# Kernel tuning notes

Hardware: AMD Instinct MI355X
Metric: run time of the kernel (lower is better)

The kernel has to match this reference:

```python
import jax, jax.numpy as jnp
import numpy as np

B, S, D = 2, 2048, 2048
NH, NKV, HD = 16, 4, 128
REP = NH // NKV
EPS = 1e-6
ROPE_THETA = 1e6


def setup_inputs() -> dict:
    key = jax.random.key(0)
    ks = jax.random.split(key, 6)
    x = jax.random.normal(ks[0], (B, S, D), jnp.float32)
    # real rotary embeddings: [S, HD]
    inv_freq = 1.0 / (ROPE_THETA ** (np.arange(0, HD, 2, dtype=np.float64) / HD))
    freqs = np.outer(np.arange(S, dtype=np.float64), inv_freq)
    emb = np.concatenate([freqs, freqs], axis=-1)
    cos = jnp.asarray(np.cos(emb), jnp.float32)
    sin = jnp.asarray(np.sin(emb), jnp.float32)
    scale = 1.0 / np.sqrt(D)
    Wq = jax.random.normal(ks[1], (D, NH * HD), jnp.float32) * scale   # [in, out]
    Wk = jax.random.normal(ks[2], (D, NKV * HD), jnp.float32) * scale
    Wv = jax.random.normal(ks[3], (D, NKV * HD), jnp.float32) * scale
    Wo = jax.random.normal(ks[4], (NH * HD, D), jnp.float32) * (1.0 / np.sqrt(NH * HD))
    q_norm_w = jnp.ones((HD,), jnp.float32)
    k_norm_w = jnp.ones((HD,), jnp.float32)
    return dict(x=x, cos=cos, sin=sin, Wq=Wq, Wk=Wk, Wv=Wv, Wo=Wo,
                q_norm_w=q_norm_w, k_norm_w=k_norm_w)


def _rms_norm(h, w):
    var = jnp.mean(h * h, axis=-1, keepdims=True)
    return w * (h * jax.lax.rsqrt(var + EPS))


def _rotate_half(h):
    h1, h2 = jnp.split(h, 2, axis=-1)
    return jnp.concatenate([-h2, h1], axis=-1)


def reference(x, cos, sin, Wq, Wk, Wv, Wo, q_norm_w, k_norm_w):
    b, s, _ = x.shape
    q = (x @ Wq).reshape(b, s, NH, HD)
    k = (x @ Wk).reshape(b, s, NKV, HD)
    v = (x @ Wv).reshape(b, s, NKV, HD)
    # per-head QK RMSNorm
    q = _rms_norm(q, q_norm_w)
    k = _rms_norm(k, k_norm_w)
    # RoPE: cos/sin [S,HD] -> broadcast over batch and heads
    c = cos[None, :, None, :]
    s_ = sin[None, :, None, :]
    q = q * c + _rotate_half(q) * s_
    k = k * c + _rotate_half(k) * s_
    # GQA: group q heads per kv head instead of materializing repeat_kv
    qg = q.reshape(b, s, NKV, REP, HD)
    scores = jnp.einsum('bqgrd,bkgd->bgrqk', qg, k) / np.sqrt(HD)
    causal = jnp.tril(jnp.ones((s, s), bool))  # [q,k]
    scores = jnp.where(causal, scores, -jnp.inf)
    probs = jax.nn.softmax(scores.astype(jnp.float32), axis=-1).astype(q.dtype)
    out = jnp.einsum('bgrqk,bkgd->bqgrd', probs, v).reshape(b, s, NH * HD)
    return out @ Wo
```

## Files before the change

### kernel.cpp

```cpp
#include <hip/hip_runtime.h>
#include <hip/hip_bf16.h>
#include <math.h>

#define B_ 2
#define S_ 2048
#define D_ 2048
#define NH_ 16
#define NKV_ 4
#define HD_ 128
#define EPS_ 1e-6f
#define SCALE_ 0.08838834764831845f
#define LOG2E_ 1.4426950408889634f
#define KOFF_ 2048
#define VOFF_ 2560

typedef float f32x4 __attribute__((ext_vector_type(4)));
typedef short bf16x8 __attribute__((ext_vector_type(8)));
typedef short short4v __attribute__((ext_vector_type(4)));
typedef float float4v __attribute__((ext_vector_type(4)));
typedef unsigned uint2v __attribute__((ext_vector_type(2)));
typedef unsigned uint4v __attribute__((ext_vector_type(4)));

static __device__ __forceinline__ short f2bf(float f) {
    union { float f; unsigned u; } x{f};
    unsigned r = (x.u + 0x7fff + ((x.u >> 16) & 1)) >> 16;
    return (short)r;
}
static __device__ __forceinline__ float bf2f(short s) {
    union { unsigned u; float f; } x; x.u = ((unsigned)(unsigned short)s) << 16; return x.f;
}
static __device__ __forceinline__ unsigned pack_bf2(float a, float b) {
    return __builtin_amdgcn_perm(__builtin_bit_cast(unsigned, b),
                                 __builtin_bit_cast(unsigned, a), 0x07060302u);
}

#define AS1(p) ((const __attribute__((address_space(1))) void*)(p))
#define AS3(p) ((__attribute__((address_space(3))) void*)(p))
static __device__ __forceinline__ void async16(const void* g, void* l) {
    __builtin_amdgcn_global_load_lds(AS1(g), AS3(l), 16, 0, 0);
}
#define SB_() __builtin_amdgcn_sched_barrier(0)

__global__ __launch_bounds__(256) void cast_kernel(const float* __restrict__ in,
                                                   short* __restrict__ out) {
    size_t i = ((size_t)blockIdx.x * 256 + threadIdx.x) * 4;
    float4v v = *(const float4v*)(in + i);
    short4v o; o.x = f2bf(v.x); o.y = f2bf(v.y); o.z = f2bf(v.z); o.w = f2bf(v.w);
    *(short4v*)(out + i) = o;
}

__global__ __launch_bounds__(256) void transpose_all_kernel(const float* __restrict__ Wq,
                                                            const float* __restrict__ Wk,
                                                            const float* __restrict__ Wv,
                                                            const float* __restrict__ Wo,
                                                            short* __restrict__ Wt,
                                                            short* __restrict__ Wot) {
    __shared__ float tile[64][65];
    const int bx = blockIdx.x, by = blockIdx.y;
    const float* src; short* dst; int N, nb;
    if (bx < 32)      { src = Wq; dst = Wt;                         N = 2048; nb = bx; }
    else if (bx < 40) { src = Wk; dst = Wt + (size_t)KOFF_ * 2048;  N = 512;  nb = bx - 32; }
    else if (bx < 48) { src = Wv; dst = Wt + (size_t)VOFF_ * 2048;  N = 512;  nb = bx - 40; }
    else              { src = Wo; dst = Wot;                        N = 2048; nb = bx - 48; }
    const int n0 = nb * 64, k0 = by * 64;
    const int tid = threadIdx.x;
    for (int r = 0; r < 16; ++r) {
        int k = r * 4 + (tid >> 6);
        int n = tid & 63;
        tile[k][n] = src[(size_t)(k0 + k) * N + n0 + n];
    }
    __syncthreads();
    for (int r = 0; r < 4; ++r) {
        int n  = r * 16 + (tid >> 4);
        int kk = (tid & 15) * 4;
        short4v o4;
        o4.x = f2bf(tile[kk + 0][n]); o4.y = f2bf(tile[kk + 1][n]);
        o4.z = f2bf(tile[kk + 2][n]); o4.w = f2bf(tile[kk + 3][n]);
        *(short4v*)&dst[(size_t)(n0 + n) * 2048 + k0 + kk] = o4;
    }
}

__global__ __launch_bounds__(512, 2) void gemm_oproj_kernel(const short* __restrict__ A,
                                                            const short* __restrict__ Bt,
                                                            float* __restrict__ C) {
    __shared__ __align__(16) short smem[49152];
    short* A0 = smem;
    short* A1 = smem + 8192;
    short* B0 = smem + 16384;
    short* B1 = smem + 32768;

    const int tid  = threadIdx.x;
    const int orig = blockIdx.y * 8 + blockIdx.x;
    const int swz  = (orig & 7) * 32 + (orig >> 3);
    const int bn = swz & 7, bm = swz >> 3;
    const int wave = tid >> 6, lane = tid & 63;
    const int quad = lane >> 4, l16 = lane & 15;
    const int wr = wave >> 2, wc = wave & 3;

    const short* Ag = A  + (size_t)(bm * 128) * 2048;
    const short* Bg = Bt + (size_t)(bn * 256) * 2048;

    f32x4 acc[4][4];
#pragma unroll
    for (int i = 0; i < 4; ++i)
#pragma unroll
        for (int j = 0; j < 4; ++j) acc[i][j] = (f32x4){0.f, 0.f, 0.f, 0.f};

    bf16x8 a[4][2], b0[2][2], b1[2][2];

    auto stage_half = [&](const short* gpanel, int t, int h, short* lslot) {
#pragma unroll
        for (int u = 0; u < 2; ++u) {
            int ci = u * 512 + tid;
            int r  = ci >> 3;
            int cb = ((ci & 7) * 16) ^ ((r & 7) << 4);
            async16(gpanel + (size_t)(h * 128 + r) * 2048 + t * 64 + (cb >> 1),
                    lslot + h * 8192 + ci * 8);
        }
    };

#define OLDA_(lbuf) \
    _Pragma("unroll") for (int mt = 0; mt < 4; ++mt) \
    _Pragma("unroll") for (int ks = 0; ks < 2; ++ks) { \
        int row_ = wr * 64 + mt * 16 + l16; \
        int cb_  = (ks * 64 + quad * 16) ^ ((row_ & 7) << 4); \
        a[mt][ks] = *(const bf16x8*)&(lbuf)[row_ * 64 + (cb_ >> 1)]; \
    }
#define OLDB_(lbuf, qn, breg) \
    _Pragma("unroll") for (int ntl = 0; ntl < 2; ++ntl) \
    _Pragma("unroll") for (int ks = 0; ks < 2; ++ks) { \
        int row_ = wc * 64 + (qn) * 32 + ntl * 16 + l16; \
        int cb_  = (ks * 64 + quad * 16) ^ ((row_ & 7) << 4); \
        breg[ntl][ks] = *(const bf16x8*)&(lbuf)[row_ * 64 + (cb_ >> 1)]; \
    }
#define OMFMA_(qn, breg) do { \
    __builtin_amdgcn_s_setprio(1); \
    _Pragma("unroll") for (int mt = 0; mt < 4; ++mt) \
    _Pragma("unroll") for (int ntl = 0; ntl < 2; ++ntl) \
    _Pragma("unroll") for (int ks = 0; ks < 2; ++ks) \
        acc[mt][(qn) * 2 + ntl] = __builtin_amdgcn_mfma_f32_16x16x32_bf16( \
            a[mt][ks], breg[ntl][ks], acc[mt][(qn) * 2 + ntl], 0, 0, 0); \
    __builtin_amdgcn_s_setprio(0); SB_(); __builtin_amdgcn_s_barrier(); } while (0)

    stage_half(Bg, 0, 0, B0); stage_half(Bg, 0, 1, B0);
    stage_half(Ag, 0, 0, A0);
    SB_(); asm volatile("s_waitcnt vmcnt(0)" ::: "memory");
    __builtin_amdgcn_s_barrier();

#pragma unroll 1
    for (int i = 0; i < 16; ++i) {
        const int tE = 2 * i, tO = 2 * i + 1;
        const bool more = (i < 15);

        stage_half(Ag, tO, 0, A1);
        stage_half(Bg, tO, 0, B1); stage_half(Bg, tO, 1, B1);
        OLDA_(A0); OLDB_(B0, 0, b0);
        OMFMA_(0, b0);

        if (more) {
            stage_half(Ag, tE + 2, 0, A0);
            SB_(); asm volatile("s_waitcnt vmcnt(2)" ::: "memory");
        } else {
            SB_(); asm volatile("s_waitcnt vmcnt(0)" ::: "memory");
        }
        OLDB_(B0, 1, b1);
        OMFMA_(1, b1);

        if (more) { stage_half(Bg, tE + 2, 0, B0); stage_half(Bg, tE + 2, 1, B0); }
        OLDA_(A1); OLDB_(B1, 0, b0);
        OMFMA_(0, b0);

        if (more) { SB_(); asm volatile("s_waitcnt vmcnt(0)" ::: "memory"); }
        OLDB_(B1, 1, b1);
        OMFMA_(1, b1);
    }

#pragma unroll
    for (int mt = 0; mt < 4; ++mt)
#pragma unroll
        for (int nt = 0; nt < 4; ++nt)
#pragma unroll
            for (int j = 0; j < 4; ++j) {
                int row = bm * 128 + wr * 64 + mt * 16 + quad * 4 + j;
                int col = bn * 256 + wc * 64 + nt * 16 + l16;
                C[(size_t)row * 2048 + col] = acc[mt][nt][j];
            }
#undef OLDA_
#undef OLDB_
#undef OMFMA_
}

#define QKV_ITERS 16

__global__ __launch_bounds__(512, 2) void qkv_fused_kernel(const short* __restrict__ xb,
                                                           const short* __restrict__ Wt,
                                                           const float* __restrict__ cosb,
                                                           const float* __restrict__ sinb,
                                                           const float* __restrict__ qw,
                                                           const float* __restrict__ kw,
                                                           short* __restrict__ q_rope,
                                                           short* __restrict__ k_rope,
                                                           short* __restrict__ vtr) {
    __shared__ __align__(16) short smem[65536];
    __shared__ float ss2[4][256];

    short* A0 = smem;
    short* A1 = smem + 16384;
    short* B0 = smem + 32768;
    short* B1 = smem + 49152;

    const int tid  = threadIdx.x;
    const int orig = blockIdx.y * 12 + blockIdx.x;
    const int swz  = (orig & 7) * 24 + (orig >> 3);
    const int bn = swz % 12, bm = swz / 12;
    const int wave = tid >> 6, lane = tid & 63;
    const int quad = lane >> 4, l16 = lane & 15;
    const int wr = wave >> 2, wc = wave & 3;

    const short* Ag = xb + (size_t)(bm * 256) * 2048;
    const short* Bg = Wt + (size_t)(bn * 256) * 2048;

    f32x4 acc[8][4];
#pragma unroll
    for (int i = 0; i < 8; ++i)
#pragma unroll
        for (int j = 0; j < 4; ++j) acc[i][j] = (f32x4){0.f, 0.f, 0.f, 0.f};

    bf16x8 a[4][2], b0[2][2], b1[2][2];

    auto stage_half = [&](const short* gpanel, int t, int h, short* lslot) {
#pragma unroll
        for (int u = 0; u < 2; ++u) {
            int ci = u * 512 + tid;
            int r  = ci >> 3;
            int cb = ((ci & 7) * 16) ^ ((r & 7) << 4);
            async16(gpanel + (size_t)(h * 128 + r) * 2048 + t * 64 + (cb >> 1),
                    lslot + h * 8192 + ci * 8);
        }
    };

#define LDA_(lbuf, qm) \
    _Pragma("unroll") for (int mt = 0; mt < 4; ++mt) \
    _Pragma("unroll") for (int ks = 0; ks < 2; ++ks) { \
        int row_ = wr * 128 + (qm) * 64 + mt * 16 + l16; \
        int cb_  = (ks * 64 + quad * 16) ^ ((row_ & 7) << 4); \
        a[mt][ks] = *(const bf16x8*)&(lbuf)[row_ * 64 + (cb_ >> 1)]; \
    }
#define LDB_(lbuf, qn, breg) \
    _Pragma("unroll") for (int ntl = 0; ntl < 2; ++ntl) \
    _Pragma("unroll") for (int ks = 0; ks < 2; ++ks) { \
        int row_ = wc * 64 + (qn) * 32 + ntl * 16 + l16; \
        int cb_  = (ks * 64 + quad * 16) ^ ((row_ & 7) << 4); \
        breg[ntl][ks] = *(const bf16x8*)&(lbuf)[row_ * 64 + (cb_ >> 1)]; \
    }
#define MFMA16_(qm, qn, breg) \
    _Pragma("unroll") for (int mt = 0; mt < 4; ++mt) \
    _Pragma("unroll") for (int ntl = 0; ntl < 2; ++ntl) \
    _Pragma("unroll") for (int ks = 0; ks < 2; ++ks) \
        acc[(qm) * 4 + mt][(qn) * 2 + ntl] = __builtin_amdgcn_mfma_f32_16x16x32_bf16( \
            a[mt][ks], breg[ntl][ks], acc[(qm) * 4 + mt][(qn) * 2 + ntl], 0, 0, 0);
#define PH_MFMA2_(qm) do { \
        __builtin_amdgcn_s_setprio(1); MFMA16_(qm, 0, b0); MFMA16_(qm, 1, b1); \
        __builtin_amdgcn_s_setprio(0); SB_(); __builtin_amdgcn_s_barrier(); } while (0)

    stage_half(Bg, 0, 0, B0); stage_half(Bg, 0, 1, B0);
    stage_half(Ag, 0, 0, A0); stage_half(Ag, 0, 1, A0);
    stage_half(Bg, 1, 0, B1); stage_half(Bg, 1, 1, B1);
    SB_(); asm volatile("s_waitcnt vmcnt(4)" ::: "memory");
    __builtin_amdgcn_s_barrier();

#pragma unroll 1
    for (int i = 0; i < QKV_ITERS; ++i) {
        const int tE = 2 * i, tO = 2 * i + 1;
        const bool more = (i < QKV_ITERS - 1);

        stage_half(Ag, tO, 0, A1); stage_half(Ag, tO, 1, A1);
        LDA_(A0, 0); LDB_(B0, 0, b0); LDB_(B0, 1, b1);
        PH_MFMA2_(0);

        if (more) {
            stage_half(Bg, tE + 2, 0, B0); stage_half(Bg, tE + 2, 1, B0);
            SB_(); asm volatile("s_waitcnt vmcnt(4)" ::: "memory");
        } else {
            SB_(); asm volatile("s_waitcnt vmcnt(0)" ::: "memory");
        }
        LDA_(A0, 1);
        PH_MFMA2_(1);

        if (more) { stage_half(Ag, tE + 2, 0, A0); stage_half(Ag, tE + 2, 1, A0); }
        LDA_(A1, 0); LDB_(B1, 0, b0); LDB_(B1, 1, b1);
        PH_MFMA2_(0);

        if (more) {
            stage_half(Bg, tO + 2, 0, B1); stage_half(Bg, tO + 2, 1, B1);
            SB_(); asm volatile("s_waitcnt vmcnt(4)" ::: "memory");
        }
        LDA_(A1, 1);
        PH_MFMA2_(1);
    }

    if (bn >= 10) {
        const int gbase = (bn - 10) * 2;
#pragma unroll
        for (int am = 0; am < 8; ++am) {
            int tok0 = bm * 256 + wr * 128 + am * 16 + quad * 4;
            int bb = tok0 >> 11, s0 = tok0 & (S_ - 1);
#pragma unroll
            for (int nt = 0; nt < 4; ++nt) {
                int col = wc * 64 + nt * 16 + l16;
                int g = gbase + (col >> 7);
                int d = col & 127;
                short4v o4;
                o4.x = f2bf(acc[am][nt][0]); o4.y = f2bf(acc[am][nt][1]);
                o4.z = f2bf(acc[am][nt][2]); o4.w = f2bf(acc[am][nt][3]);
                *(short4v*)&vtr[((size_t)(bb * NKV_ + g) * HD_ + d) * S_ + s0] = o4;
            }
        }
        return;
    }

    {
        float pss[8][4];
#pragma unroll
        for (int am = 0; am < 8; ++am)
#pragma unroll
            for (int j = 0; j < 4; ++j) {
                float s = 0.f;
#pragma unroll
                for (int nt = 0; nt < 4; ++nt) s += acc[am][nt][j] * acc[am][nt][j];
                pss[am][j] = s;
            }
#pragma unroll
        for (int off = 1; off < 16; off <<= 1)
#pragma unroll
            for (int am = 0; am < 8; ++am)
#pragma unroll
                for (int j = 0; j < 4; ++j)
                    pss[am][j] += __shfl_xor(pss[am][j], off);
        if (l16 == 0)
#pragma unroll
            for (int am = 0; am < 8; ++am)
#pragma unroll
                for (int j = 0; j < 4; ++j)
                    ss2[wc][wr * 128 + am * 16 + quad * 4 + j] = pss[am][j];
    }
    short* ct = smem;
#pragma unroll
    for (int am = 0; am < 8; ++am)
#pragma unroll
        for (int nt = 0; nt < 4; ++nt)
#pragma unroll
            for (int j = 0; j < 4; ++j)
                ct[(wr * 128 + am * 16 + quad * 4 + j) * 256 + wc * 64 + nt * 16 + l16]
                    = f2bf(acc[am][nt][j]);
    __syncthreads();

    const bool isQ = (bn < 8);
    const float osc = isQ ? (SCALE_ * LOG2E_) : 1.0f;
    const float* w = isQ ? qw : kw;
#pragma unroll 1
    for (int it = 0; it < 16; ++it) {
        int idx = it * 512 + tid;
        int row = idx >> 5;
        int s32 = idx & 31;
        int head = s32 >> 4, seg = s32 & 15;
        int tok = bm * 256 + row;
        int bb = tok >> 11, s = tok & (S_ - 1);
        float rstd = rsqrtf((ss2[2 * head][row] + ss2[2 * head + 1][row]) * (1.0f / HD_) + EPS_);
        int c0 = seg * 8, p0 = (seg ^ 8) * 8;
        bf16x8 ta = *(const bf16x8*)&ct[row * 256 + head * 128 + c0];
        bf16x8 tb = *(const bf16x8*)&ct[row * 256 + head * 128 + p0];
        float sgn = (seg < 8) ? -1.0f : 1.0f;
        float4v cs0 = *(const float4v*)&cosb[(size_t)s * HD_ + c0];
        float4v cs1 = *(const float4v*)&cosb[(size_t)s * HD_ + c0 + 4];
        float4v sn0 = *(const float4v*)&sinb[(size_t)s * HD_ + c0];
        float4v sn1 = *(const float4v*)&sinb[(size_t)s * HD_ + c0 + 4];
        float ov[8];
#pragma unroll
        for (int i = 0; i < 8; ++i) {
            float n1 = bf2f(ta[i]) * rstd * w[c0 + i];
            float n2 = bf2f(tb[i]) * rstd * w[p0 + i];
            float cs = (i < 4) ? cs0[i & 3] : cs1[i & 3];
            float sn = (i < 4) ? sn0[i & 3] : sn1[i & 3];
            ov[i] = (n1 * cs + sgn * n2 * sn) * osc;
        }
        uint4v wv;
#pragma unroll
        for (int i2 = 0; i2 < 4; ++i2)
            wv[i2] = ((unsigned)(unsigned short)f2bf(ov[2 * i2])) |
                     ((unsigned)(unsigned short)f2bf(ov[2 * i2 + 1]) << 16);
        int gh = isQ ? (bn * 2 + head) : ((bn - 8) * 2 + head);
        short* dst = isQ
            ? q_rope + ((size_t)(bb * S_ + s) * NH_ + gh) * HD_ + c0
            : k_rope + ((size_t)(bb * NKV_ + gh) * S_ + s) * HD_ + c0;
        *(uint4v*)dst = wv;
    }
#undef LDA_
#undef LDB_
#undef MFMA16_
#undef PH_MFMA2_
}

__global__ __launch_bounds__(256, 2) void attn_kernel(const short* __restrict__ qr,
                                                      const short* __restrict__ kg,
                                                      const short* __restrict__ vt,
                                                      short* __restrict__ aout) {
    __shared__ short Ks[2][64 * 128];
    __shared__ short Vs[2][128 * 64];

    const int lin = blockIdx.x;
    const int b  = lin & 1;
    const int g  = (lin >> 1) & 3;
    const int hq = (lin >> 3) & 3;
    const int pr = lin >> 5;
    const int h  = g * 4 + hq;

    const int wave = threadIdx.x >> 6, lane = threadIdx.x & 63;
    const int quad = lane >> 4, l16 = lane & 15;

    const short* kbase = kg + (size_t)(b * NKV_ + g) * S_ * HD_;
    const short* vbase = vt + (size_t)(b * NKV_ + g) * HD_ * S_;

    for (int pass = 0; pass < 2; ++pass) {
        const int qt    = pass ? (31 - pr) : pr;
        const int iters = qt + 1;
        const int qrow  = qt * 64 + wave * 16 + l16;

        bf16x8 qf[4];
        {
            const short* qp = qr + ((size_t)(b * S_ + qrow) * NH_ + h) * HD_;
            for (int ks = 0; ks < 4; ++ks)
                qf[ks] = *(const bf16x8*)(qp + ks * 32 + quad * 8);
        }

        f32x4 o[8];
        for (int i = 0; i < 8; ++i) o[i] = (f32x4){0.f, 0.f, 0.f, 0.f};
        float m_i = -INFINITY, l_i = 0.f;

        auto stage = [&](int kt, int bsel) {
            const short* kt_base = kbase + (size_t)kt * 64 * HD_;
            const short* vt_base = vbase + kt * 64;
            for (int t = 0; t < 4; ++t) {
                int ci  = (wave * 4 + t) * 64 + lane;
                int key = ci >> 4;
                int c   = (ci & 15) ^ ((key ^ (key >> 2)) & 15);
                async16(kt_base + key * HD_ + c * 8, &Ks[bsel][ci * 8]);
            }
            for (int t = 0; t < 4; ++t) {
                int ci = (wave * 4 + t) * 64 + lane;
                int d  = ci >> 3;
                int c  = (ci & 7) ^ (d & 7);
                async16(vt_base + (size_t)d * S_ + c * 8, &Vs[bsel][ci * 8]);
            }
        };

        stage(0, 0);
        int buf = 0;
        for (int kt = 0; kt < iters; ++kt) {
            __syncthreads();
            if (kt + 1 < iters) stage(kt + 1, buf ^ 1);

            f32x4 acc[4];
            for (int t = 0; t < 4; ++t) acc[t] = (f32x4){0.f, 0.f, 0.f, 0.f};
            __builtin_amdgcn_s_setprio(1);
            for (int t = 0; t < 4; ++t) {
                int lk = ((t >> 1) << 5) + ((l16 >> 2) << 3) + ((t & 1) << 2) + (l16 & 3);
                const short* kp = &Ks[buf][lk * 128];
                int pm = (lk ^ (lk >> 2)) & 15;
                for (int ks = 0; ks < 4; ++ks) {
                    bf16x8 kf = *(const bf16x8*)(kp + (((ks * 4 + quad) ^ pm) * 8));
                    acc[t] = __builtin_amdgcn_mfma_f32_16x16x32_bf16(kf, qf[ks], acc[t], 0, 0, 0);
                }
            }
            __builtin_amdgcn_s_setprio(0);
            const int key_base = kt * 64;
            if (key_base + 63 > qt * 64 + wave * 16) {
                for (int t = 0; t < 4; ++t)
                    for (int j = 0; j < 4; ++j) {
                        int kl = key_base + ((t >> 1) << 5) + (quad << 3) + ((t & 1) << 2) + j;
                        if (kl > qrow) acc[t][j] = -INFINITY;
                    }
            }
            float mx = m_i;
            for (int t = 0; t < 4; ++t)
                for (int j = 0; j < 4; ++j) mx = fmaxf(mx, acc[t][j]);
            mx = fmaxf(mx, __shfl_xor(mx, 16));
            mx = fmaxf(mx, __shfl_xor(mx, 32));
            float al = __builtin_amdgcn_exp2f(m_i - mx);
            m_i = mx;
            float rs = 0.f;
            float p[4][4];
            for (int t = 0; t < 4; ++t)
                for (int j = 0; j < 4; ++j) {
                    float e = __builtin_amdgcn_exp2f(acc[t][j] - mx);
                    p[t][j] = e;
                    rs += e;
                }
            rs += __shfl_xor(rs, 16);
            rs += __shfl_xor(rs, 32);
            l_i = al * l_i + rs;
            for (int d8 = 0; d8 < 8; ++d8)
                for (int j = 0; j < 4; ++j) o[d8][j] *= al;
            unsigned pk[2][4];
            for (int grp = 0; grp < 2; ++grp) {
                pk[grp][0] = pack_bf2(p[2 * grp][0],     p[2 * grp][1]);
                pk[grp][1] = pack_bf2(p[2 * grp][2],     p[2 * grp][3]);
                pk[grp][2] = pack_bf2(p[2 * grp + 1][0], p[2 * grp + 1][1]);
                pk[grp][3] = pack_bf2(p[2 * grp + 1][2], p[2 * grp + 1][3]);
            }
            __builtin_amdgcn_s_setprio(1);
            for (int grp = 0; grp < 2; ++grp) {
                union { unsigned u[4]; bf16x8 v; } pb;
                for (int i = 0; i < 4; ++i) pb.u[i] = pk[grp][i];
                for (int d8 = 0; d8 < 8; ++d8) {
                    int d = d8 * 16 + l16;
                    bf16x8 vf = *(const bf16x8*)&Vs[buf][d * 64 + (((grp * 4 + quad) ^ (d & 7)) * 8)];
                    o[d8] = __builtin_amdgcn_mfma_f32_16x16x32_bf16(vf, pb.v, o[d8], 0, 0, 0);
                }
            }
            __builtin_amdgcn_s_setprio(0);
            buf ^= 1;
        }
        float il = 1.0f / l_i;
        short* op = aout + ((size_t)(b * S_ + qrow) * NH_ + h) * HD_ + quad * 4;
        for (int d8 = 0; d8 < 8; ++d8) {
            uint2v wv;
            wv.x = ((unsigned)(unsigned short)f2bf(o[d8][0] * il)) |
                   ((unsigned)(unsigned short)f2bf(o[d8][1] * il) << 16);
            wv.y = ((unsigned)(unsigned short)f2bf(o[d8][2] * il)) |
                   ((unsigned)(unsigned short)f2bf(o[d8][3] * il) << 16);
            *(uint2v*)(op + d8 * 16) = wv;
        }
        __syncthreads();
    }
}

extern "C" void kernel_launch(void* const* d_in, const int* in_sizes, int n_in,
                              void* d_out, int out_size, void* d_ws, size_t ws_size,
                              hipStream_t stream) {
    (void)in_sizes; (void)n_in; (void)out_size; (void)ws_size;
    const float* x    = (const float*)d_in[0];
    const float* cosb = (const float*)d_in[1];
    const float* sinb = (const float*)d_in[2];
    const float* Wq   = (const float*)d_in[3];
    const float* Wk   = (const float*)d_in[4];
    const float* Wv   = (const float*)d_in[5];
    const float* Wo   = (const float*)d_in[6];
    const float* qw   = (const float*)d_in[7];
    const float* kw   = (const float*)d_in[8];
    float* out = (float*)d_out;

    char* ws = (char*)d_ws;
    short* xb     = (short*)ws;  ws += (size_t)4096 * 2048 * 2;
    short* Wt     = (short*)ws;  ws += (size_t)3072 * 2048 * 2;
    short* Wot    = (short*)ws;  ws += (size_t)2048 * 2048 * 2;
    short* q_rope = (short*)ws;  ws += (size_t)4096 * 2048 * 2;
    short* k_rope = (short*)ws;  ws += (size_t)4096 * 512 * 2;
    short* vt     = (short*)ws;  ws += (size_t)4096 * 512 * 2;
    short* a_out  = (short*)ws;  ws += (size_t)4096 * 2048 * 2;

    const int M = B_ * S_;

    cast_kernel<<<M * 2048 / 1024, 256, 0, stream>>>(x, xb);
    transpose_all_kernel<<<dim3(80, 32), 256, 0, stream>>>(Wq, Wk, Wv, Wo, Wt, Wot);

    qkv_fused_kernel<<<dim3(12, M / 256), 512, 0, stream>>>(
        xb, Wt, cosb, sinb, qw, kw, q_rope, k_rope, vt);

    attn_kernel<<<512, 256, 0, stream>>>(q_rope, k_rope, vt, a_out);

    gemm_oproj_kernel<<<dim3(8, 32), 512, 0, stream>>>(a_out, Wot, out);
}
```

Measured before the change: 292.6 us.

## Double query rows per attention wave and reschedule GEMM barriers and LDS loads

The attention kernel now processes two 64-row query sub-tiles per wave (128-row tiles), so each K/V tile loaded into LDS feeds twice as many MFMAs. Grid size halves and launch bounds drop to one block per SIMD group to make room for the extra registers. The QKV GEMM moves its LDS fragment loads ahead of global staging and uses sched_barrier-fenced workgroup barriers, and the O-projection GEMM adds an extra barrier before each MFMA phase. Register pressure rises and occupancy falls, and the added barriers may cost synchronization time.

```diff
diff --git a/kernel.cpp b/kernel.cpp
--- a/kernel.cpp
+++ b/kernel.cpp
@@ -133,6 +133,7 @@
         int cb_  = (ks * 64 + quad * 16) ^ ((row_ & 7) << 4); \
         breg[ntl][ks] = *(const bf16x8*)&(lbuf)[row_ * 64 + (cb_ >> 1)]; \
     }
+#define OBAR_() do { SB_(); __builtin_amdgcn_s_barrier(); } while (0)
 #define OMFMA_(qn, breg) do { \
     __builtin_amdgcn_s_setprio(1); \
     _Pragma("unroll") for (int mt = 0; mt < 4; ++mt) \
@@ -155,6 +156,7 @@
         stage_half(Ag, tO, 0, A1);
         stage_half(Bg, tO, 0, B1); stage_half(Bg, tO, 1, B1);
         OLDA_(A0); OLDB_(B0, 0, b0);
+        OBAR_();
         OMFMA_(0, b0);
 
         if (more) {
@@ -164,14 +166,17 @@
             SB_(); asm volatile("s_waitcnt vmcnt(0)" ::: "memory");
         }
         OLDB_(B0, 1, b1);
+        OBAR_();
         OMFMA_(1, b1);
 
         if (more) { stage_half(Bg, tE + 2, 0, B0); stage_half(Bg, tE + 2, 1, B0); }
         OLDA_(A1); OLDB_(B1, 0, b0);
+        OBAR_();
         OMFMA_(0, b0);
 
         if (more) { SB_(); asm volatile("s_waitcnt vmcnt(0)" ::: "memory"); }
         OLDB_(B1, 1, b1);
+        OBAR_();
         OMFMA_(1, b1);
     }
 
@@ -187,6 +192,7 @@
             }
 #undef OLDA_
 #undef OLDB_
+#undef OBAR_
 #undef OMFMA_
 }
 
@@ -259,14 +265,16 @@
     _Pragma("unroll") for (int ks = 0; ks < 2; ++ks) \
         acc[(qm) * 4 + mt][(qn) * 2 + ntl] = __builtin_amdgcn_mfma_f32_16x16x32_bf16( \
             a[mt][ks], breg[ntl][ks], acc[(qm) * 4 + mt][(qn) * 2 + ntl], 0, 0, 0);
-#define PH_MFMA2_(qm) do { \
+#define PH_BAR() do { __builtin_amdgcn_sched_barrier(0); __builtin_amdgcn_s_barrier(); } while (0)
+#define PH_MFMA2(qm) do { \
         __builtin_amdgcn_s_setprio(1); MFMA16_(qm, 0, b0); MFMA16_(qm, 1, b1); \
-        __builtin_amdgcn_s_setprio(0); SB_(); __builtin_amdgcn_s_barrier(); } while (0)
+        __builtin_amdgcn_s_setprio(0); \
+        __builtin_amdgcn_sched_barrier(0); __builtin_amdgcn_s_barrier(); } while (0)
 
     stage_half(Bg, 0, 0, B0); stage_half(Bg, 0, 1, B0);
     stage_half(Ag, 0, 0, A0); stage_half(Ag, 0, 1, A0);
     stage_half(Bg, 1, 0, B1); stage_half(Bg, 1, 1, B1);
-    SB_(); asm volatile("s_waitcnt vmcnt(4)" ::: "memory");
+    asm volatile("s_waitcnt vmcnt(4)" ::: "memory");
     __builtin_amdgcn_s_barrier();
 
 #pragma unroll 1
@@ -274,29 +282,33 @@
         const int tE = 2 * i, tO = 2 * i + 1;
         const bool more = (i < QKV_ITERS - 1);
 
+        LDA_(A0, 0); LDB_(B0, 0, b0); LDB_(B0, 1, b1);
         stage_half(Ag, tO, 0, A1); stage_half(Ag, tO, 1, A1);
-        LDA_(A0, 0); LDB_(B0, 0, b0); LDB_(B0, 1, b1);
-        PH_MFMA2_(0);
-
+        PH_BAR();
+        PH_MFMA2(0);
+
+        LDA_(A0, 1);
         if (more) {
             stage_half(Bg, tE + 2, 0, B0); stage_half(Bg, tE + 2, 1, B0);
-            SB_(); asm volatile("s_waitcnt vmcnt(4)" ::: "memory");
+            asm volatile("s_waitcnt vmcnt(4)" ::: "memory");
         } else {
-            SB_(); asm volatile("s_waitcnt vmcnt(0)" ::: "memory");
-        }
-        LDA_(A0, 1);
-        PH_MFMA2_(1);
-
+            asm volatile("s_waitcnt vmcnt(0)" ::: "memory");
+        }
+        PH_BAR();
+        PH_MFMA2(1);
+
+        LDA_(A1, 0); LDB_(B1, 0, b0); LDB_(B1, 1, b1);
         if (more) { stage_half(Ag, tE + 2, 0, A0); stage_half(Ag, tE + 2, 1, A0); }
-        LDA_(A1, 0); LDB_(B1, 0, b0); LDB_(B1, 1, b1);
-        PH_MFMA2_(0);
-
+        PH_BAR();
+        PH_MFMA2(0);
+
+        LDA_(A1, 1);
         if (more) {
             stage_half(Bg, tO + 2, 0, B1); stage_half(Bg, tO + 2, 1, B1);
-            SB_(); asm volatile("s_waitcnt vmcnt(4)" ::: "memory");
-        }
-        LDA_(A1, 1);
-        PH_MFMA2_(1);
+            asm volatile("s_waitcnt vmcnt(4)" ::: "memory");
+        }
+        PH_BAR();
+        PH_MFMA2(1);
     }
 
     if (bn >= 10) {
@@ -398,10 +410,11 @@
 #undef LDA_
 #undef LDB_
 #undef MFMA16_
-#undef PH_MFMA2_
-}
-
-__global__ __launch_bounds__(256, 2) void attn_kernel(const short* __restrict__ qr,
+#undef PH_BAR
+#undef PH_MFMA2
+}
+
+__global__ __launch_bounds__(256, 1) void attn_kernel(const short* __restrict__ qr,
                                                       const short* __restrict__ kg,
                                                       const short* __restrict__ vt,
                                                       short* __restrict__ aout) {
@@ -422,20 +435,27 @@
     const short* vbase = vt + (size_t)(b * NKV_ + g) * HD_ * S_;
 
     for (int pass = 0; pass < 2; ++pass) {
-        const int qt    = pass ? (31 - pr) : pr;
-        const int iters = qt + 1;
-        const int qrow  = qt * 64 + wave * 16 + l16;
-
-        bf16x8 qf[4];
-        {
-            const short* qp = qr + ((size_t)(b * S_ + qrow) * NH_ + h) * HD_;
+        const int qt    = pass ? (15 - pr) : pr;
+        const int iters = 2 * qt + 2;
+        int qrow0 = qt * 128 + wave * 16 + l16;
+        int qrow1 = qrow0 + 64;
+
+        bf16x8 qf[2][4];
+#pragma unroll
+        for (int qs = 0; qs < 2; ++qs) {
+            const short* qp = qr + ((size_t)(b * S_ + (qs ? qrow1 : qrow0)) * NH_ + h) * HD_;
+#pragma unroll
             for (int ks = 0; ks < 4; ++ks)
-                qf[ks] = *(const bf16x8*)(qp + ks * 32 + quad * 8);
-        }
-
-        f32x4 o[8];
-        for (int i = 0; i < 8; ++i) o[i] = (f32x4){0.f, 0.f, 0.f, 0.f};
-        float m_i = -INFINITY, l_i = 0.f;
+                qf[qs][ks] = *(const bf16x8*)(qp + ks * 32 + quad * 8);
+        }
+
+        f32x4 o[2][8];
+#pragma unroll
+        for (int qs = 0; qs < 2; ++qs)
+#pragma unroll
+            for (int i = 0; i < 8; ++i) o[qs][i] = (f32x4){0.f, 0.f, 0.f, 0.f};
+        float m_i[2] = {-INFINITY, -INFINITY};
+        float l_i[2] = {0.f, 0.f};
 
         auto stage = [&](int kt, int bsel) {
             const short* kt_base = kbase + (size_t)kt * 64 * HD_;
@@ -460,76 +480,108 @@
             __syncthreads();
             if (kt + 1 < iters) stage(kt + 1, buf ^ 1);
 
-            f32x4 acc[4];
-            for (int t = 0; t < 4; ++t) acc[t] = (f32x4){0.f, 0.f, 0.f, 0.f};
+            f32x4 acc[2][4];
+#pragma unroll
+            for (int qs = 0; qs < 2; ++qs)
+#pragma unroll
+                for (int t = 0; t < 4; ++t) acc[qs][t] = (f32x4){0.f, 0.f, 0.f, 0.f};
             __builtin_amdgcn_s_setprio(1);
+#pragma unroll
             for (int t = 0; t < 4; ++t) {
                 int lk = ((t >> 1) << 5) + ((l16 >> 2) << 3) + ((t & 1) << 2) + (l16 & 3);
                 const short* kp = &Ks[buf][lk * 128];
                 int pm = (lk ^ (lk >> 2)) & 15;
+#pragma unroll
                 for (int ks = 0; ks < 4; ++ks) {
                     bf16x8 kf = *(const bf16x8*)(kp + (((ks * 4 + quad) ^ pm) * 8));
-                    acc[t] = __builtin_amdgcn_mfma_f32_16x16x32_bf16(kf, qf[ks], acc[t], 0, 0, 0);
+                    acc[0][t] = __builtin_amdgcn_mfma_f32_16x16x32_bf16(kf, qf[0][ks], acc[0][t], 0, 0, 0);
+                    acc[1][t] = __builtin_amdgcn_mfma_f32_16x16x32_bf16(kf, qf[1][ks], acc[1][t], 0, 0, 0);
                 }
             }
             __builtin_amdgcn_s_setprio(0);
             const int key_base = kt * 64;
-            if (key_base + 63 > qt * 64 + wave * 16) {
+#pragma unroll
+            for (int qs = 0; qs < 2; ++qs) {
+                int qmin = qt * 128 + qs * 64 + wave * 16;
+                int qrow = qs ? qrow1 : qrow0;
+                if (key_base + 63 > qmin) {
+#pragma unroll
+                    for (int t = 0; t < 4; ++t)
+#pragma unroll
+                        for (int j = 0; j < 4; ++j) {
+                            int kl = key_base + ((t >> 1) << 5) + (quad << 3) + ((t & 1) << 2) + j;
+                            if (kl > qrow) acc[qs][t][j] = -INFINITY;
+                        }
+                }
+            }
+            unsigned pk[2][2][4];
+#pragma unroll
+            for (int qs = 0; qs < 2; ++qs) {
+                float mx = m_i[qs];
+#pragma unroll
                 for (int t = 0; t < 4; ++t)
+#pragma unroll
+                    for (int j = 0; j < 4; ++j) mx = fmaxf(mx, acc[qs][t][j]);
+                mx = fmaxf(mx, __shfl_xor(mx, 16));
+                mx = fmaxf(mx, __shfl_xor(mx, 32));
+                float al = __builtin_amdgcn_exp2f(m_i[qs] - mx);
+                m_i[qs] = mx;
+                float rs = 0.f;
+                float p[4][4];
+#pragma unroll
+                for (int t = 0; t < 4; ++t)
+#pragma unroll
                     for (int j = 0; j < 4; ++j) {
-                        int kl = key_base + ((t >> 1) << 5) + (quad << 3) + ((t & 1) << 2) + j;
-                        if (kl > qrow) acc[t][j] = -INFINITY;
+                        float e = __builtin_amdgcn_exp2f(acc[qs][t][j] - mx);
+                        p[t][j] = e;
+                        rs += e;
                     }
-            }
-            float mx = m_i;
-            for (int t = 0; t < 4; ++t)
-                for (int j = 0; j < 4; ++j) mx = fmaxf(mx, acc[t][j]);
-            mx = fmaxf(mx, __shfl_xor(mx, 16));
-            mx = fmaxf(mx, __shfl_xor(mx, 32));
-            float al = __builtin_amdgcn_exp2f(m_i - mx);
-            m_i = mx;
-            float rs = 0.f;
-            float p[4][4];
-            for (int t = 0; t < 4; ++t)
-                for (int j = 0; j < 4; ++j) {
-                    float e = __builtin_amdgcn_exp2f(acc[t][j] - mx);
-                    p[t][j] = e;
-                    rs += e;
+                rs += __shfl_xor(rs, 16);
+                rs += __shfl_xor(rs, 32);
+                l_i[qs] = al * l_i[qs] + rs;
+#pragma unroll
+                for (int d8 = 0; d8 < 8; ++d8)
+#pragma unroll
+                    for (int j = 0; j < 4; ++j) o[qs][d8][j] *= al;
+#pragma unroll
+                for (int grp = 0; grp < 2; ++grp) {
+                    pk[qs][grp][0] = pack_bf2(p[2 * grp][0],     p[2 * grp][1]);
+                    pk[qs][grp][1] = pack_bf2(p[2 * grp][2],     p[2 * grp][3]);
+                    pk[qs][grp][2] = pack_bf2(p[2 * grp + 1][0], p[2 * grp + 1][1]);
+                    pk[qs][grp][3] = pack_bf2(p[2 * grp + 1][2], p[2 * grp + 1][3]);
                 }
-            rs += __shfl_xor(rs, 16);
-            rs += __shfl_xor(rs, 32);
-            l_i = al * l_i + rs;
-            for (int d8 = 0; d8 < 8; ++d8)
-                for (int j = 0; j < 4; ++j) o[d8][j] *= al;
-            unsigned pk[2][4];
+            }
+            __builtin_amdgcn_s_setprio(1);
+#pragma unroll
             for (int grp = 0; grp < 2; ++grp) {
-                pk[grp][0] = pack_bf2(p[2 * grp][0],     p[2 * grp][1]);
-                pk[grp][1] = pack_bf2(p[2 * grp][2],     p[2 * grp][3]);
-                pk[grp][2] = pack_bf2(p[2 * grp + 1][0], p[2 * grp + 1][1]);
-                pk[grp][3] = pack_bf2(p[2 * grp + 1][2], p[2 * grp + 1][3]);
-            }
-            __builtin_amdgcn_s_setprio(1);
-            for (int grp = 0; grp < 2; ++grp) {
-                union { unsigned u[4]; bf16x8 v; } pb;
-                for (int i = 0; i < 4; ++i) pb.u[i] = pk[grp][i];
+                union { unsigned u[4]; bf16x8 v; } pb0, pb1;
+#pragma unroll
+                for (int i = 0; i < 4; ++i) { pb0.u[i] = pk[0][grp][i]; pb1.u[i] = pk[1][grp][i]; }
+#pragma unroll
                 for (int d8 = 0; d8 < 8; ++d8) {
                     int d = d8 * 16 + l16;
                     bf16x8 vf = *(const bf16x8*)&Vs[buf][d * 64 + (((grp * 4 + quad) ^ (d & 7)) * 8)];
-                    o[d8] = __builtin_amdgcn_mfma_f32_16x16x32_bf16(vf, pb.v, o[d8], 0, 0, 0);
+                    o[0][d8] = __builtin_amdgcn_mfma_f32_16x16x32_bf16(vf, pb0.v, o[0][d8], 0, 0, 0);
+                    o[1][d8] = __builtin_amdgcn_mfma_f32_16x16x32_bf16(vf, pb1.v, o[1][d8], 0, 0, 0);
                 }
             }
             __builtin_amdgcn_s_setprio(0);
             buf ^= 1;
         }
-        float il = 1.0f / l_i;
-        short* op = aout + ((size_t)(b * S_ + qrow) * NH_ + h) * HD_ + quad * 4;
-        for (int d8 = 0; d8 < 8; ++d8) {
-            uint2v wv;
-            wv.x = ((unsigned)(unsigned short)f2bf(o[d8][0] * il)) |
-                   ((unsigned)(unsigned short)f2bf(o[d8][1] * il) << 16);
-            wv.y = ((unsigned)(unsigned short)f2bf(o[d8][2] * il)) |
-                   ((unsigned)(unsigned short)f2bf(o[d8][3] * il) << 16);
-            *(uint2v*)(op + d8 * 16) = wv;
+#pragma unroll
+        for (int qs = 0; qs < 2; ++qs) {
+            float il = 1.0f / l_i[qs];
+            int qrow = qs ? qrow1 : qrow0;
+            short* op = aout + ((size_t)(b * S_ + qrow) * NH_ + h) * HD_ + quad * 4;
+#pragma unroll
+            for (int d8 = 0; d8 < 8; ++d8) {
+                uint2v wv;
+                wv.x = ((unsigned)(unsigned short)f2bf(o[qs][d8][0] * il)) |
+                       ((unsigned)(unsigned short)f2bf(o[qs][d8][1] * il) << 16);
+                wv.y = ((unsigned)(unsigned short)f2bf(o[qs][d8][2] * il)) |
+                       ((unsigned)(unsigned short)f2bf(o[qs][d8][3] * il) << 16);
+                *(uint2v*)(op + d8 * 16) = wv;
+            }
         }
         __syncthreads();
     }
@@ -567,7 +619,7 @@
     qkv_fused_kernel<<<dim3(12, M / 256), 512, 0, stream>>>(
         xb, Wt, cosb, sinb, qw, kw, q_rope, k_rope, vt);
 
-    attn_kernel<<<512, 256, 0, stream>>>(q_rope, k_rope, vt, a_out);
+    attn_kernel<<<256, 256, 0, stream>>>(q_rope, k_rope, vt, a_out);
 
     gemm_oproj_kernel<<<dim3(8, 32), 512, 0, stream>>>(a_out, Wot, out);
 }
```

Measured after the change: 312.5 us. 6.8% more time.
